# Kernel optimization log

Measured on AMD Instinct MI355X. Metric: run time of the kernel, lower is better.

## Reference

```python
import jax, jax.numpy as jnp
import numpy as np

NEG_BIG = 1e9


def setup_inputs() -> dict:
    key = jax.random.key(0)
    k1, k2, k3, k4 = jax.random.split(key, 4)
    B, N, M, D = 4, 512, 512, 128
    x = jax.random.normal(k1, (B, N, D), dtype=jnp.float32)
    y = jax.random.normal(k2, (B, M, D), dtype=jnp.float32)
    # lengths in [64, 512] so every example has a non-empty alignment region
    x_length = jax.random.randint(k3, (B,), 64, N + 1, dtype=jnp.int64)
    y_length = jax.random.randint(k4, (B,), 64, M + 1, dtype=jnp.int64)
    return {"x": x, "y": y, "x_length": x_length, "y_length": y_length}


def reference(x, y, x_length, y_length):
    B, N, D = x.shape
    M = y.shape[1]
    # sequence masks from lengths
    x_mask = jnp.arange(N)[None, :] < x_length[:, None]          # [B, N]
    y_mask = jnp.arange(M)[None, :] < y_length[:, None]          # [B, M]
    attention_mask = (x_mask[:, :, None] & y_mask[:, None, :]).astype(x.dtype)  # [B, N, M]
    # pairwise L1 distance: [B, N, M]
    z_diff = jnp.sum(jnp.abs(x[:, :, None, :] - y[:, None, :, :]), axis=-1)
    weights = -z_diff - NEG_BIG * (1.0 - attention_mask)
    alpha = jax.nn.softmax(weights, axis=1)  # over x positions
    beta = jax.nn.softmax(weights, axis=2)   # over y positions
    a = attention_mask * (alpha + beta - alpha * beta)
    ssa = -jnp.sum(a * z_diff, axis=(1, 2)) / jnp.sum(a, axis=(1, 2))  # [B]
    return ssa
```

## Files before the change

### kernel.cpp

```cpp
#include <hip/hip_runtime.h>


constexpr int B = 4, N = 512, M = 512, D = 128;
constexpr int TN = 64, TM = 64;
constexpr int LSTR = D + 4;
constexpr int NSLOT = 16;
#define SENT -3.0e38f

__device__ __forceinline__ int load_len(const int* p, int b) {
  bool is64 = (p[1] == 0) && (p[3] == 0);
  return is64 ? p[2 * b] : p[b];
}

__device__ __forceinline__ void compute_tile(const float* __restrict__ x,
                                             const float* __restrict__ y,
                                             int b, int n0, int m0, int tid,
                                             float* xs, float* ys,
                                             float zr[4][4]) {
  const float4* xg = (const float4*)(x + (size_t)(b * N + n0) * D);
  const float4* yg = (const float4*)(y + (size_t)(b * M + m0) * D);
#pragma unroll
  for (int k = 0; k < 8; ++k) {
    int idx = tid + k * 256;
    int r = idx >> 5;
    int c = (idx & 31) << 2;
    *(float4*)&xs[r * LSTR + c] = xg[idx];
    *(float4*)&ys[r * LSTR + c] = yg[idx];
  }
  __syncthreads();

  const int tx = tid & 15;
  const int ty = tid >> 4;
#pragma unroll
  for (int i = 0; i < 4; ++i)
#pragma unroll
    for (int j = 0; j < 4; ++j) zr[i][j] = 0.f;

#pragma unroll 4
  for (int dd = 0; dd < D; dd += 4) {
    float4 xa[4], yb[4];
#pragma unroll
    for (int i = 0; i < 4; ++i) xa[i] = *(const float4*)&xs[(ty + 16 * i) * LSTR + dd];
#pragma unroll
    for (int j = 0; j < 4; ++j) yb[j] = *(const float4*)&ys[(tx + 16 * j) * LSTR + dd];
#pragma unroll
    for (int i = 0; i < 4; ++i)
#pragma unroll
      for (int j = 0; j < 4; ++j) {
        zr[i][j] += fabsf(xa[i].x - yb[j].x);
        zr[i][j] += fabsf(xa[i].y - yb[j].y);
        zr[i][j] += fabsf(xa[i].z - yb[j].z);
        zr[i][j] += fabsf(xa[i].w - yb[j].w);
      }
  }
}

__global__ __launch_bounds__(256) void k1_stats(const float* __restrict__ x,
                                                const float* __restrict__ y,
                                                const int* __restrict__ xlen,
                                                const int* __restrict__ ylen,
                                                float2* __restrict__ rp,
                                                float2* __restrict__ cp,
                                                float* __restrict__ acc) {
  __shared__ float xs[TN * LSTR];
  __shared__ float ys[TM * LSTR];
  __shared__ float2 colp[4][TM];
  const int b  = blockIdx.z;
  const int n0 = blockIdx.y * TN;
  const int m0 = blockIdx.x * TM;
  const int tid = threadIdx.x;
  const int xl = load_len(xlen, b);
  const int yl = load_len(ylen, b);

  if (blockIdx.x == 0 && blockIdx.y == 0 && blockIdx.z == 0 && tid < 2 * B * NSLOT)
    acc[tid] = 0.f;

  float zr[4][4];
  compute_tile(x, y, b, n0, m0, tid, xs, ys, zr);

  const int tx = tid & 15;
  const int ty = tid >> 4;
  const int wv = tid >> 6;

#pragma unroll
  for (int i = 0; i < 4; ++i) {
    float lm = SENT;
#pragma unroll
    for (int j = 0; j < 4; ++j)
      if (m0 + tx + 16 * j < yl) lm = fmaxf(lm, -zr[i][j]);
#pragma unroll
    for (int off = 1; off <= 8; off <<= 1) lm = fmaxf(lm, __shfl_xor(lm, off, 64));
    float ls = 0.f;
#pragma unroll
    for (int j = 0; j < 4; ++j)
      if (m0 + tx + 16 * j < yl) ls += __expf(-zr[i][j] - lm);
#pragma unroll
    for (int off = 1; off <= 8; off <<= 1) ls += __shfl_xor(ls, off, 64);
    if (tx == 0)
      rp[((b * 8 + (m0 >> 6)) * N) + n0 + ty + 16 * i] = make_float2(lm, ls);
  }

#pragma unroll
  for (int j = 0; j < 4; ++j) {
    float cm = SENT;
#pragma unroll
    for (int i = 0; i < 4; ++i)
      if (n0 + ty + 16 * i < xl) cm = fmaxf(cm, -zr[i][j]);
    cm = fmaxf(cm, __shfl_xor(cm, 16, 64));
    cm = fmaxf(cm, __shfl_xor(cm, 32, 64));
    float cs = 0.f;
#pragma unroll
    for (int i = 0; i < 4; ++i)
      if (n0 + ty + 16 * i < xl) cs += __expf(-zr[i][j] - cm);
    cs += __shfl_xor(cs, 16, 64);
    cs += __shfl_xor(cs, 32, 64);
    if ((ty & 3) == 0) colp[wv][tx + 16 * j] = make_float2(cm, cs);
  }
  __syncthreads();
  if (tid < TM) {
    float2 p0 = colp[0][tid], p1 = colp[1][tid], p2 = colp[2][tid], p3 = colp[3][tid];
    float gm = fmaxf(fmaxf(p0.x, p1.x), fmaxf(p2.x, p3.x));
    float gs = p0.y * __expf(p0.x - gm) + p1.y * __expf(p1.x - gm) +
               p2.y * __expf(p2.x - gm) + p3.y * __expf(p3.x - gm);
    cp[((b * 8 + (n0 >> 6)) * M) + m0 + tid] = make_float2(gm, gs);
  }
}

__global__ __launch_bounds__(256) void k2_final(const float* __restrict__ x,
                                                const float* __restrict__ y,
                                                const int* __restrict__ xlen,
                                                const int* __restrict__ ylen,
                                                const float2* __restrict__ rp,
                                                const float2* __restrict__ cp,
                                                float* __restrict__ acc) {
  __shared__ float xs[TN * LSTR];
  __shared__ float ys[TM * LSTR];
  __shared__ float rm_s[TN], ri_s[TN], cm_s[TM], ci_s[TM];
  __shared__ float red[4][2];
  const int b  = blockIdx.z;
  const int n0 = blockIdx.y * TN;
  const int m0 = blockIdx.x * TM;
  const int tid = threadIdx.x;
  const int xl = load_len(xlen, b);
  const int yl = load_len(ylen, b);

  if (tid < 128) {
    bool isrow = tid < 64;
    int p = isrow ? (n0 + tid) : (m0 + tid - 64);
    const float2* src = isrow ? rp : cp;
    float2 v[8];
    float gm = SENT;
#pragma unroll
    for (int t = 0; t < 8; ++t) {
      v[t] = src[(b * 8 + t) * 512 + p];
      gm = fmaxf(gm, v[t].x);
    }
    float gs = 0.f;
#pragma unroll
    for (int t = 0; t < 8; ++t) gs += v[t].y * __expf(v[t].x - gm);
    float inv = 1.0f / gs;
    if (isrow) { rm_s[tid] = gm; ri_s[tid] = inv; }
    else       { cm_s[tid - 64] = gm; ci_s[tid - 64] = inv; }
  }

  float zr[4][4];
  compute_tile(x, y, b, n0, m0, tid, xs, ys, zr);

  const int tx = tid & 15;
  const int ty = tid >> 4;
  float num = 0.f, den = 0.f;
#pragma unroll
  for (int i = 0; i < 4; ++i) {
    int nl = ty + 16 * i;
    if (n0 + nl >= xl) continue;
    float rm = rm_s[nl], ri = ri_s[nl];
#pragma unroll
    for (int j = 0; j < 4; ++j) {
      int ml = tx + 16 * j;
      if (m0 + ml >= yl) continue;
      float zv = zr[i][j];
      float w = -zv;
      float alpha = __expf(w - cm_s[ml]) * ci_s[ml];
      float beta  = __expf(w - rm) * ri;
      float a = alpha + beta - alpha * beta;
      num += a * zv;
      den += a;
    }
  }
#pragma unroll
  for (int off = 32; off > 0; off >>= 1) {
    num += __shfl_xor(num, off, 64);
    den += __shfl_xor(den, off, 64);
  }
  __syncthreads();
  if ((tid & 63) == 0) { red[tid >> 6][0] = num; red[tid >> 6][1] = den; }
  __syncthreads();
  if (tid == 0) {
    int slot = (blockIdx.x + blockIdx.y) & (NSLOT - 1);
    atomicAdd(&acc[b * NSLOT + slot],
              red[0][0] + red[1][0] + red[2][0] + red[3][0]);
    atomicAdd(&acc[(B + b) * NSLOT + slot],
              red[0][1] + red[1][1] + red[2][1] + red[3][1]);
  }
}

__global__ void k3_out(const float* __restrict__ acc, float* __restrict__ out) {
  int l = threadIdx.x;
  float a = acc[l];
  float d = acc[64 + l];
#pragma unroll
  for (int off = 1; off <= 8; off <<= 1) {
    a += __shfl_xor(a, off, 64);
    d += __shfl_xor(d, off, 64);
  }
  if ((l & 15) == 0) out[l >> 4] = -a / d;
}

extern "C" void kernel_launch(void* const* d_in, const int* in_sizes, int n_in,
                              void* d_out, int out_size, void* d_ws, size_t ws_size,
                              hipStream_t stream) {
  const float* x    = (const float*)d_in[0];
  const float* y    = (const float*)d_in[1];
  const int*   xlen = (const int*)d_in[2];
  const int*   ylen = (const int*)d_in[3];
  float* out = (float*)d_out;

  float* ws = (float*)d_ws;
  float2* rp  = (float2*)ws;              size_t off = (size_t)B * 8 * N * 2;
  float2* cp  = (float2*)(ws + off);      off += (size_t)B * 8 * M * 2;
  float*  acc = ws + off;                 off += 2 * B * NSLOT;

  k1_stats<<<dim3(M / TM, N / TN, B), 256, 0, stream>>>(x, y, xlen, ylen, rp, cp, acc);
  k2_final<<<dim3(M / TM, N / TN, B), 256, 0, stream>>>(x, y, xlen, ylen, rp, cp, acc);
  k3_out<<<1, 64, 0, stream>>>(acc, out);
}
```

Baseline: 92.61 us.

## Store distance tiles in k1 and reuse them in k2 instead of recomputing

The first kernel now writes its 64x64 per-tile L1 distance values to a global workspace buffer. The second kernel reads them back instead of reloading x and y and recomputing the distances, which removes half of the O(N*M*D) compute and all of k2's shared memory. In exchange it adds 4 MB of global writes and reads, plus a larger workspace requirement.

```diff
diff --git a/kernel.cpp b/kernel.cpp
--- a/kernel.cpp
+++ b/kernel.cpp
@@ -61,7 +61,8 @@
                                                 const int* __restrict__ ylen,
                                                 float2* __restrict__ rp,
                                                 float2* __restrict__ cp,
-                                                float* __restrict__ acc) {
+                                                float* __restrict__ acc,
+                                                float* __restrict__ zt_all) {
   __shared__ float xs[TN * LSTR];
   __shared__ float ys[TM * LSTR];
   __shared__ float2 colp[4][TM];
@@ -78,6 +79,12 @@
   float zr[4][4];
   compute_tile(x, y, b, n0, m0, tid, xs, ys, zr);
 
+  float* zt = zt_all + ((size_t)((b * 8 + (n0 >> 6)) * 8 + (m0 >> 6))) * (TN * TM);
+#pragma unroll
+  for (int i = 0; i < 4; ++i)
+    *(float4*)&zt[(i * 256 + tid) * 4] =
+        make_float4(zr[i][0], zr[i][1], zr[i][2], zr[i][3]);
+
   const int tx = tid & 15;
   const int ty = tid >> 4;
   const int wv = tid >> 6;
@@ -126,15 +133,12 @@
   }
 }
 
-__global__ __launch_bounds__(256) void k2_final(const float* __restrict__ x,
-                                                const float* __restrict__ y,
-                                                const int* __restrict__ xlen,
+__global__ __launch_bounds__(256) void k2_final(const int* __restrict__ xlen,
                                                 const int* __restrict__ ylen,
                                                 const float2* __restrict__ rp,
                                                 const float2* __restrict__ cp,
+                                                const float* __restrict__ zt_all,
                                                 float* __restrict__ acc) {
-  __shared__ float xs[TN * LSTR];
-  __shared__ float ys[TM * LSTR];
   __shared__ float rm_s[TN], ri_s[TN], cm_s[TM], ci_s[TM];
   __shared__ float red[4][2];
   const int b  = blockIdx.z;
@@ -144,6 +148,11 @@
   const int xl = load_len(xlen, b);
   const int yl = load_len(ylen, b);
 
+  const float* zt = zt_all + ((size_t)((b * 8 + (n0 >> 6)) * 8 + (m0 >> 6))) * (TN * TM);
+  float4 zv[4];
+#pragma unroll
+  for (int i = 0; i < 4; ++i) zv[i] = *(const float4*)&zt[(i * 256 + tid) * 4];
+
   if (tid < 128) {
     bool isrow = tid < 64;
     int p = isrow ? (n0 + tid) : (m0 + tid - 64);
@@ -162,9 +171,7 @@
     if (isrow) { rm_s[tid] = gm; ri_s[tid] = inv; }
     else       { cm_s[tid - 64] = gm; ci_s[tid - 64] = inv; }
   }
-
-  float zr[4][4];
-  compute_tile(x, y, b, n0, m0, tid, xs, ys, zr);
+  __syncthreads();
 
   const int tx = tid & 15;
   const int ty = tid >> 4;
@@ -174,16 +181,17 @@
     int nl = ty + 16 * i;
     if (n0 + nl >= xl) continue;
     float rm = rm_s[nl], ri = ri_s[nl];
+    float zrow[4] = {zv[i].x, zv[i].y, zv[i].z, zv[i].w};
 #pragma unroll
     for (int j = 0; j < 4; ++j) {
       int ml = tx + 16 * j;
       if (m0 + ml >= yl) continue;
-      float zv = zr[i][j];
-      float w = -zv;
+      float zval = zrow[j];
+      float w = -zval;
       float alpha = __expf(w - cm_s[ml]) * ci_s[ml];
       float beta  = __expf(w - rm) * ri;
       float a = alpha + beta - alpha * beta;
-      num += a * zv;
+      num += a * zval;
       den += a;
     }
   }
@@ -192,7 +200,6 @@
     num += __shfl_xor(num, off, 64);
     den += __shfl_xor(den, off, 64);
   }
-  __syncthreads();
   if ((tid & 63) == 0) { red[tid >> 6][0] = num; red[tid >> 6][1] = den; }
   __syncthreads();
   if (tid == 0) {
@@ -229,8 +236,9 @@
   float2* rp  = (float2*)ws;              size_t off = (size_t)B * 8 * N * 2;
   float2* cp  = (float2*)(ws + off);      off += (size_t)B * 8 * M * 2;
   float*  acc = ws + off;                 off += 2 * B * NSLOT;
-
-  k1_stats<<<dim3(M / TM, N / TN, B), 256, 0, stream>>>(x, y, xlen, ylen, rp, cp, acc);
-  k2_final<<<dim3(M / TM, N / TN, B), 256, 0, stream>>>(x, y, xlen, ylen, rp, cp, acc);
+  float*  zt  = ws + off;                 off += (size_t)B * 8 * 8 * TN * TM;
+
+  k1_stats<<<dim3(M / TM, N / TN, B), 256, 0, stream>>>(x, y, xlen, ylen, rp, cp, acc, zt);
+  k2_final<<<dim3(M / TM, N / TN, B), 256, 0, stream>>>(xlen, ylen, rp, cp, zt, acc);
   k3_out<<<1, 64, 0, stream>>>(acc, out);
 }
```

Result: faster. 82.72 us (-10.7%).
